# Kernel optimization log

Hardware: AMD Instinct MI355X
Metric: run time of the kernel (lower is better)

## Reference

```python
import jax, jax.numpy as jnp
import numpy as np

B_, L_, D_MODEL, N_LAYER, VOCAB = 4, 2048, 512, 2, 128
D_INNER, D_STATE, DT_RANK, D_CONV = 2 * D_MODEL, 16, D_MODEL // 16, 4
NDIR = 2  # forward / backward Mamba stacks


def setup_inputs() -> dict:
    key = jax.random.key(0)
    ks = jax.random.split(key, 12)
    f = jax.random.normal
    A_init = jnp.broadcast_to(
        jnp.log(jnp.arange(1, D_STATE + 1, dtype=jnp.float32)),
        (NDIR, N_LAYER, D_INNER, D_STATE)) + 0.0
    return {
        "input_ids": jax.random.randint(ks[0], (B_, L_), 0, VOCAB),
        "padding_mask": jnp.ones((B_, L_), dtype=bool),
        "embed": 0.02 * f(ks[1], (NDIR, VOCAB, D_MODEL)),
        "in_proj_w": 0.02 * f(ks[2], (NDIR, N_LAYER, 2 * D_INNER, D_MODEL)),
        "conv_w": 0.1 * f(ks[3], (NDIR, N_LAYER, D_INNER, 1, D_CONV)),
        "conv_b": 0.1 * f(ks[4], (NDIR, N_LAYER, D_INNER)),
        "x_proj_w": 0.02 * f(ks[5], (NDIR, N_LAYER, DT_RANK + 2 * D_STATE, D_INNER)),
        "dt_proj_w": 0.1 * f(ks[6], (NDIR, N_LAYER, D_INNER, DT_RANK)),
        "dt_proj_b": -4.0 + 0.5 * jax.random.uniform(ks[7], (NDIR, N_LAYER, D_INNER)),
        "A_log": A_init,
        "D": jnp.ones((NDIR, N_LAYER, D_INNER)),
        "out_proj_w": 0.02 * f(ks[8], (NDIR, N_LAYER, D_MODEL, D_INNER)),
        "norm_w": jnp.ones((NDIR, N_LAYER, D_MODEL)),
        "norm_f_w": jnp.ones((NDIR, D_MODEL)),
        "proj_w": 0.02 * f(ks[9], (D_MODEL, 2 * D_MODEL)),
        "proj_b": jnp.zeros((D_MODEL,)),
    }


def _rmsnorm(x, w, eps=1e-5):
    return x * jax.lax.rsqrt(jnp.mean(jnp.square(x), axis=-1, keepdims=True) + eps) * w


def _selective_scan(u, dt, Bm, Cm, A, Dp):
    # u, dt: (b, l, d_inner); Bm, Cm: (b, l, d_state)
    b, l, di = u.shape

    def step(h, inp):
        u_t, dt_t, b_t, c_t = inp                      # (b,di) (b,di) (b,n) (b,n)
        dA = jnp.exp(dt_t[:, :, None] * A)             # (b, di, n)
        h = dA * h + (dt_t * u_t)[:, :, None] * b_t[:, None, :]
        return h, jnp.einsum('bdn,bn->bd', h, c_t)

    h0 = jnp.zeros((b, di, A.shape[-1]), u.dtype)
    xs = (jnp.swapaxes(u, 0, 1), jnp.swapaxes(dt, 0, 1),
          jnp.swapaxes(Bm, 0, 1), jnp.swapaxes(Cm, 0, 1))
    _, ys = jax.lax.scan(step, h0, xs)                 # ys: (l, b, di)
    return jnp.swapaxes(ys, 0, 1) + u * Dp


def _mamba(x, p):
    in_w, cw, cb, xw, dtw, dtb, alog, dp, ow = p
    xz = jnp.einsum('bld,ed->ble', x, in_w)            # (b, l, 2*d_inner)
    u, z = jnp.split(xz, 2, axis=-1)
    uc = jnp.swapaxes(u, 1, 2)                         # (b, d_inner, l)
    uc = jax.lax.conv_general_dilated(
        uc, cw, (1,), [(D_CONV - 1, 0)], feature_group_count=D_INNER)
    u = jax.nn.silu(jnp.swapaxes(uc + cb[None, :, None], 1, 2))
    xdbl = jnp.einsum('bld,ed->ble', u, xw)
    dt, Bm, Cm = jnp.split(xdbl, [DT_RANK, DT_RANK + D_STATE], axis=-1)
    dt = jax.nn.softplus(jnp.einsum('blr,dr->bld', dt, dtw) + dtb)
    y = _selective_scan(u, dt, Bm, Cm, -jnp.exp(alog), dp)
    y = y * jax.nn.silu(z)
    return jnp.einsum('bld,ed->ble', y, ow)


def _mixer(ids, d, embed, in_proj_w, conv_w, conv_b, x_proj_w, dt_proj_w,
           dt_proj_b, A_log, D, out_proj_w, norm_w, norm_f_w):
    hidden = embed[d][ids]
    residual = None
    for i in range(N_LAYER):
        residual = hidden if residual is None else hidden + residual
        hidden = _rmsnorm(residual, norm_w[d, i])
        p = (in_proj_w[d, i], conv_w[d, i], conv_b[d, i], x_proj_w[d, i],
             dt_proj_w[d, i], dt_proj_b[d, i], A_log[d, i], D[d, i],
             out_proj_w[d, i])
        hidden = _mamba(hidden, p)
    return _rmsnorm(hidden + residual, norm_f_w[d])


def reference(input_ids, padding_mask, embed, in_proj_w, conv_w, conv_b,
              x_proj_w, dt_proj_w, dt_proj_b, A_log, D, out_proj_w, norm_w,
              norm_f_w, proj_w, proj_b):
    args = (embed, in_proj_w, conv_w, conv_b, x_proj_w, dt_proj_w, dt_proj_b,
            A_log, D, out_proj_w, norm_w, norm_f_w)
    fwd = _mixer(input_ids, 0, *args)
    bwd = jnp.flip(_mixer(jnp.flip(input_ids, 1), 1, *args), 1)
    out = jnp.concatenate([fwd, bwd], axis=-1)        # (b, l, 2*d_model)
    return jnp.einsum('ble,oe->blo', out, proj_w) + proj_b
```

## Files before the change

### kernel.cpp

```cpp
#include <hip/hip_runtime.h>
#include <hip/hip_bf16.h>

#define B_   4
#define L_   2048
#define DM   512
#define DI   1024
#define NST  16
#define DTR  32
#define ROWS  (B_ * L_)
#define ROWS2 (2 * ROWS)
#define NCHUNK 32
#define CLEN  (L_ / NCHUNK)
#define LN2R 1.4426950408889634f

typedef unsigned short u16;
typedef __attribute__((ext_vector_type(8))) short bf16x8;
typedef __attribute__((ext_vector_type(4))) float f32x4;
typedef __attribute__((ext_vector_type(4))) float float4v;
typedef __attribute__((ext_vector_type(2))) float f32x2;

__device__ __forceinline__ float bf2f(u16 h) {
  union { unsigned int u; float f; } v; v.u = ((unsigned int)h) << 16; return v.f;
}
__device__ __forceinline__ u16 f2bf(float f) {
  union { float f; unsigned int u; } v; v.f = f;
  unsigned int u = v.u;
  if ((u & 0x7fffffffu) > 0x7f800000u) return (u16)((u >> 16) | 0x0040u);
  return (u16)((u + 0x7fffu + ((u >> 16) & 1u)) >> 16);
}
__device__ __forceinline__ float sigmoidf_(float x) { return 1.f / (1.f + __expf(-x)); }

__device__ __forceinline__ f32x2 pk_mul(f32x2 a, f32x2 b) {
  f32x2 d; asm("v_pk_mul_f32 %0, %1, %2" : "=v"(d) : "v"(a), "v"(b)); return d;
}
__device__ __forceinline__ f32x2 pk_fma(f32x2 a, f32x2 b, f32x2 c) {
  f32x2 d; asm("v_pk_fma_f32 %0, %1, %2, %3" : "=v"(d) : "v"(a), "v"(b), "v"(c)); return d;
}

__device__ __forceinline__ void gload16(const u16* g, u16* l) {
  __builtin_amdgcn_global_load_lds(
      (const __attribute__((address_space(1))) void*)g,
      (__attribute__((address_space(3))) void*)l, 16, 0, 0);
}

__global__ __launch_bounds__(256) void cvt_k(const float* __restrict__ in,
                                             u16* __restrict__ out, int n4) {
  int i = blockIdx.x * 256 + threadIdx.x;
  if (i >= n4) return;
  float4v v = *(const float4v*)&in[i * 4];
  u16 o[4];
  o[0] = f2bf(v.x); o[1] = f2bf(v.y); o[2] = f2bf(v.z); o[3] = f2bf(v.w);
  *(ulong1*)&out[i * 4] = *(ulong1*)o;
}

__global__ __launch_bounds__(256) void trp_k(const float* __restrict__ in,
                                             float* __restrict__ out) {
  int o = blockIdx.x * 256 + threadIdx.x;
  int li = o >> 15;
  int k = (o >> 10) & (DTR - 1);
  int d = o & (DI - 1);
  out[o] = in[((size_t)li * DI + d) * DTR + k];
}

__global__ __launch_bounds__(256) void embed_k(const int* __restrict__ ids,
                                               const float* __restrict__ emb,
                                               float* __restrict__ res) {
  int idx = blockIdx.x * 256 + threadIdx.x;
  int c = idx & (DM - 1);
  int row = idx >> 9;
  int dir = row >> 13;
  int r = row & (ROWS - 1);
  int b = r >> 11;
  int l = r & (L_ - 1);
  int sl = dir ? (L_ - 1 - l) : l;
  int id = ids[(b << 11) + sl];
  res[idx] = emb[(size_t)dir * 128 * DM + id * DM + c];
}

template <bool ADD>
__global__ __launch_bounds__(256) void addnorm_k(float* __restrict__ res,
                                                 const float* __restrict__ hid,
                                                 const float* __restrict__ norm_w,
                                                 int layer,
                                                 u16* __restrict__ xn) {
  int row = blockIdx.x;
  int dir = row >> 13;
  const float* w = norm_w + (size_t)(dir * 2 + layer) * DM;
  int tid = threadIdx.x;
  int base = row * DM;
  float x0 = res[base + tid];
  float x1 = res[base + 256 + tid];
  if (ADD) {
    x0 += hid[base + tid];
    x1 += hid[base + 256 + tid];
    res[base + tid] = x0;
    res[base + 256 + tid] = x1;
  }
  float s = x0 * x0 + x1 * x1;
  for (int off = 32; off; off >>= 1) s += __shfl_xor(s, off);
  __shared__ float ps[4];
  if (!(tid & 63)) ps[tid >> 6] = s;
  __syncthreads();
  float tot = ps[0] + ps[1] + ps[2] + ps[3];
  float rs = 1.f / sqrtf(tot / (float)DM + 1e-5f);
  xn[base + tid]       = f2bf(x0 * rs * w[tid]);
  xn[base + 256 + tid] = f2bf(x1 * rs * w[tid + 256]);
}

#define MFMA_B16(a, b, c) __builtin_amdgcn_mfma_f32_16x16x32_bf16(a, b, c, 0, 0, 0)

__global__ __launch_bounds__(512) void gemm8p_k(const u16* __restrict__ A,
                                                const u16* __restrict__ W,
                                                u16* __restrict__ outU,
                                                u16* __restrict__ outZ,
                                                int K) {
  __shared__ u16 As[2][2][256 * 32];
  __shared__ u16 Wsh[2][2][256 * 32];
  int tid = threadIdx.x;
  int lane = tid & 63;
  int wv = tid >> 6;
  int wr = wv >> 2, wc = wv & 3;
  int bid = blockIdx.x;
  int xcd = bid & 7, jj = bid >> 3;
  int mt = xcd * 8 + (jj & 7);
  int nt = jj >> 3;
  int m0 = mt * 256, n0 = nt * 256;
  const u16* Weff = W + (size_t)(m0 >> 13) * (size_t)2 * (2 * DI) * DM;
  f32x4 acc[8][4];
#pragma unroll
  for (int i = 0; i < 8; ++i)
#pragma unroll
    for (int j = 0; j < 4; ++j) acc[i][j] = (f32x4){0.f, 0.f, 0.f, 0.f};
  int rr = lane & 15;
  int sl = lane >> 4;
  int pofs = ((sl + (rr >> 1)) & 3) * 8;
  int lr = lane >> 2;
  int ls = ((lane & 3) - (lr >> 1)) & 3;

  auto stA = [&](int tau, int ks) {
    int buf = tau & 1;
#pragma unroll
    for (int j = 0; j < 2; ++j)
      gload16(A + (size_t)(m0 + j * 128 + wv * 16 + lr) * K + tau * 64 + ks * 32 + ls * 8,
              &As[buf][ks][(j * 128 + wv * 16) * 32]);
  };
  auto stW = [&](int tau, int ks) {
    int buf = tau & 1;
#pragma unroll
    for (int j = 0; j < 2; ++j)
      gload16(Weff + (size_t)(n0 + j * 128 + wv * 16 + lr) * K + tau * 64 + ks * 32 + ls * 8,
              &Wsh[buf][ks][(j * 128 + wv * 16) * 32]);
  };

  int NT = K / 64;
  stA(0, 0); stW(0, 0); stA(0, 1); stW(0, 1);
  asm volatile("s_waitcnt vmcnt(4)" ::: "memory");
  __builtin_amdgcn_sched_barrier(0);
  __builtin_amdgcn_s_barrier();
  __builtin_amdgcn_sched_barrier(0);

  for (int tau = 0; tau < NT; ++tau) {
    int buf = tau & 1;
    bool more = (tau + 1 < NT);
    bf16x8 af[8], w0, w1;
#pragma unroll
    for (int mi = 0; mi < 8; ++mi)
      af[mi] = *(bf16x8*)&As[buf][0][(wr * 128 + mi * 16 + rr) * 32 + pofs];
    w0 = *(bf16x8*)&Wsh[buf][0][(wc * 64 + 0 * 16 + rr) * 32 + pofs];
    w1 = *(bf16x8*)&Wsh[buf][0][(wc * 64 + 1 * 16 + rr) * 32 + pofs];
    if (more) stA(tau + 1, 0);
    __builtin_amdgcn_sched_barrier(0);
    __builtin_amdgcn_s_barrier();
    asm volatile("s_waitcnt lgkmcnt(0)" ::: "memory");
    __builtin_amdgcn_sched_barrier(0);
    __builtin_amdgcn_s_setprio(1);
#pragma unroll
    for (int mi = 0; mi < 8; ++mi) {
      acc[mi][0] = MFMA_B16(af[mi], w0, acc[mi][0]);
      acc[mi][1] = MFMA_B16(af[mi], w1, acc[mi][1]);
    }
    __builtin_amdgcn_s_setprio(0);
    __builtin_amdgcn_s_barrier();
    __builtin_amdgcn_sched_barrier(0);
    w0 = *(bf16x8*)&Wsh[buf][0][(wc * 64 + 2 * 16 + rr) * 32 + pofs];
    w1 = *(bf16x8*)&Wsh[buf][0][(wc * 64 + 3 * 16 + rr) * 32 + pofs];
    if (more) {
      stW(tau + 1, 0);
      asm volatile("s_waitcnt vmcnt(4)" ::: "memory");
    } else {
      asm volatile("s_waitcnt vmcnt(0)" ::: "memory");
    }
    __builtin_amdgcn_sched_barrier(0);
    __builtin_amdgcn_s_barrier();
    asm volatile("s_waitcnt lgkmcnt(0)" ::: "memory");
    __builtin_amdgcn_sched_barrier(0);
    __builtin_amdgcn_s_setprio(1);
#pragma unroll
    for (int mi = 0; mi < 8; ++mi) {
      acc[mi][2] = MFMA_B16(af[mi], w0, acc[mi][2]);
      acc[mi][3] = MFMA_B16(af[mi], w1, acc[mi][3]);
    }
    __builtin_amdgcn_s_setprio(0);
    __builtin_amdgcn_s_barrier();
    __builtin_amdgcn_sched_barrier(0);
#pragma unroll
    for (int mi = 0; mi < 8; ++mi)
      af[mi] = *(bf16x8*)&As[buf][1][(wr * 128 + mi * 16 + rr) * 32 + pofs];
    w0 = *(bf16x8*)&Wsh[buf][1][(wc * 64 + 0 * 16 + rr) * 32 + pofs];
    w1 = *(bf16x8*)&Wsh[buf][1][(wc * 64 + 1 * 16 + rr) * 32 + pofs];
    if (more) stA(tau + 1, 1);
    __builtin_amdgcn_sched_barrier(0);
    __builtin_amdgcn_s_barrier();
    asm volatile("s_waitcnt lgkmcnt(0)" ::: "memory");
    __builtin_amdgcn_sched_barrier(0);
    __builtin_amdgcn_s_setprio(1);
#pragma unroll
    for (int mi = 0; mi < 8; ++mi) {
      acc[mi][0] = MFMA_B16(af[mi], w0, acc[mi][0]);
      acc[mi][1] = MFMA_B16(af[mi], w1, acc[mi][1]);
    }
    __builtin_amdgcn_s_setprio(0);
    __builtin_amdgcn_s_barrier();
    __builtin_amdgcn_sched_barrier(0);
    w0 = *(bf16x8*)&Wsh[buf][1][(wc * 64 + 2 * 16 + rr) * 32 + pofs];
    w1 = *(bf16x8*)&Wsh[buf][1][(wc * 64 + 3 * 16 + rr) * 32 + pofs];
    if (more) {
      stW(tau + 1, 1);
      asm volatile("s_waitcnt vmcnt(4)" ::: "memory");
    }
    __builtin_amdgcn_sched_barrier(0);
    __builtin_amdgcn_s_barrier();
    asm volatile("s_waitcnt lgkmcnt(0)" ::: "memory");
    __builtin_amdgcn_sched_barrier(0);
    __builtin_amdgcn_s_setprio(1);
#pragma unroll
    for (int mi = 0; mi < 8; ++mi) {
      acc[mi][2] = MFMA_B16(af[mi], w0, acc[mi][2]);
      acc[mi][3] = MFMA_B16(af[mi], w1, acc[mi][3]);
    }
    __builtin_amdgcn_s_setprio(0);
    __builtin_amdgcn_s_barrier();
    __builtin_amdgcn_sched_barrier(0);
  }
  int cr = (lane >> 4) << 2;
  int cc = lane & 15;
  u16* outp = (n0 < DI) ? outU : outZ;
  int cb0 = (n0 < DI) ? n0 : (n0 - DI);
#pragma unroll
  for (int mi = 0; mi < 8; ++mi)
#pragma unroll
    for (int ni = 0; ni < 4; ++ni) {
      int row = m0 + wr * 128 + mi * 16 + cr;
      int col = cb0 + wc * 64 + ni * 16 + cc;
#pragma unroll
      for (int j = 0; j < 4; ++j)
        outp[(size_t)(row + j) * DI + col] = f2bf(acc[mi][ni][j]);
    }
}

#define EPI_F32  0
#define EPI_BF16 1
#define EPI_BIAS 2

template <int BN, int EPI, int SK = 1>
__global__ __launch_bounds__(256) void gemm_bt(const u16* __restrict__ A,
                                               const u16* __restrict__ W,
                                               void* __restrict__ outp,
                                               const float* __restrict__ bias,
                                               int N, int K, size_t wsd) {
  constexpr int BM = 128, BK = 32;
  constexpr int NF = BN / 32;
  constexpr int G = (BN == 128) ? 4 : 3;
  __shared__ u16 As[4][BM * BK];
  __shared__ u16 Wsh[4][BN * BK];
  int tid = threadIdx.x;
  int lane = tid & 63;
  int wv = tid >> 6;
  int wr = wv >> 1, wc = wv & 1;
  int m0 = blockIdx.x * BM;
  int n0 = (SK > 1) ? 0 : blockIdx.y * BN;
  int koff = (SK > 1) ? blockIdx.y * (K / SK) : 0;
  int KS = K / SK;
  int NK = KS / BK;
  const u16* Weff = W + (size_t)(m0 >> 13) * wsd;
  f32x4 acc[4][NF];
#pragma unroll
  for (int i = 0; i < 4; ++i)
#pragma unroll
    for (int j = 0; j < NF; ++j) acc[i][j] = (f32x4){0.f, 0.f, 0.f, 0.f};
  int rr = lane & 15;
  int kk = (lane >> 4) << 3;
  int l4 = lane >> 2;
  int c8 = (lane & 3) << 3;
  const u16* Ag = A + (size_t)(m0 + l4) * K + koff + c8;
  const u16* Wg = Weff + (size_t)(n0 + l4) * K + koff + c8;

  auto stage = [&](int k0, int buf) {
    gload16(Ag + (size_t)(wv * 16) * K + k0, &As[buf][wv * 512]);
    gload16(Ag + (size_t)((wv + 4) * 16) * K + k0, &As[buf][(wv + 4) * 512]);
    gload16(Wg + (size_t)(wv * 16) * K + k0, &Wsh[buf][wv * 512]);
    if (BN == 128)
      gload16(Wg + (size_t)((wv + 4) * 16) * K + k0, &Wsh[buf][(wv + 4) * 512]);
  };

  stage(0, 0); stage(BK, 1); stage(2 * BK, 2);
  for (int k = 0; k < NK; ++k) {
    if (k < NK - 2)
      asm volatile("s_waitcnt vmcnt(%0)" :: "n"(2 * G) : "memory");
    else if (k == NK - 2)
      asm volatile("s_waitcnt vmcnt(%0)" :: "n"(G) : "memory");
    else
      asm volatile("s_waitcnt vmcnt(0)" ::: "memory");
    __builtin_amdgcn_s_barrier();
    __builtin_amdgcn_sched_barrier(0);
    if (k + 3 < NK) stage((k + 3) * BK, (k + 3) & 3);
    __builtin_amdgcn_sched_barrier(0);
    int cur = k & 3;
    bf16x8 af[4], wf[NF];
#pragma unroll
    for (int mi = 0; mi < 4; ++mi)
      af[mi] = *(bf16x8*)&As[cur][(wr * 64 + mi * 16 + rr) * BK + kk];
#pragma unroll
    for (int ni = 0; ni < NF; ++ni)
      wf[ni] = *(bf16x8*)&Wsh[cur][(wc * (BN / 2) + ni * 16 + rr) * BK + kk];
#pragma unroll
    for (int mi = 0; mi < 4; ++mi)
#pragma unroll
      for (int ni = 0; ni < NF; ++ni)
        acc[mi][ni] = __builtin_amdgcn_mfma_f32_16x16x32_bf16(af[mi], wf[ni], acc[mi][ni], 0, 0, 0);
  }
  int cr = (lane >> 4) << 2;
  int cc = lane & 15;
  float* outF = (float*)outp +
      ((SK > 1) ? (size_t)blockIdx.y * (size_t)gridDim.x * BM * N : 0);
#pragma unroll
  for (int mi = 0; mi < 4; ++mi)
#pragma unroll
    for (int ni = 0; ni < NF; ++ni) {
      int row = m0 + wr * 64 + mi * 16 + cr;
      int col = n0 + wc * (BN / 2) + ni * 16 + cc;
      float bv = (EPI == EPI_BIAS) ? bias[col] : 0.f;
#pragma unroll
      for (int j = 0; j < 4; ++j) {
        float v = acc[mi][ni][j] + bv;
        if (EPI == EPI_BF16)
          ((u16*)outp)[(size_t)(row + j) * N + col] = f2bf(v);
        else
          outF[(size_t)(row + j) * N + col] = v;
      }
    }
}

__global__ __launch_bounds__(256) void conv_k(const u16* __restrict__ xzu,
                                              const float* __restrict__ conv_w,
                                              const float* __restrict__ conv_b,
                                              int layer,
                                              u16* __restrict__ uh) {
  int idx = blockIdx.x * 256 + threadIdx.x;
  int c = idx & (DI - 1);
  int row = idx >> 10;
  int dir = row >> 13;
  int l = row & (L_ - 1);
  const float* cw = conv_w + (size_t)(dir * 2 + layer) * DI * 4;
  const float* cb = conv_b + (size_t)(dir * 2 + layer) * DI;
  float acc = cb[c];
#pragma unroll
  for (int j = 0; j < 4; ++j) {
    int ls = l + j - 3;
    if (ls >= 0)
      acc += bf2f(xzu[(size_t)(row + j - 3) * DI + c]) * cw[c * 4 + j];
  }
  float s = acc * sigmoidf_(acc);
  uh[idx] = f2bf(s);
}

__device__ __forceinline__ bool a_fast(const float* alog, int d, float& a20) {
  a20 = -__expf(alog[d * NST]) * LN2R;
  bool fast = true;
#pragma unroll
  for (int n = 1; n < NST; ++n) {
    float an = -__expf(alog[d * NST + n]) * LN2R;
    fast &= (fabsf(an - (float)(n + 1) * a20) <= 1e-5f * (float)(n + 1) * fabsf(a20));
  }
  return fast;
}

__device__ __forceinline__ void stage_xs(float (*xs)[64], const float* xp,
                                         size_t rowbase, int tid) {
  size_t base = rowbase * 64;
  const float4v* s0 = (const float4v*)(xp + base);
  const float4v* s1 = (const float4v*)(xp + (size_t)ROWS2 * 64 + base);
  const float4v* s2 = (const float4v*)(xp + (size_t)2 * ROWS2 * 64 + base);
  const float4v* s3 = (const float4v*)(xp + (size_t)3 * ROWS2 * 64 + base);
  float4v* dst = (float4v*)&xs[0][0];
#pragma unroll
  for (int i = 0; i < CLEN / 16; ++i)
    dst[tid + i * 256] = s0[tid + i * 256] + s1[tid + i * 256] +
                         s2[tid + i * 256] + s3[tid + i * 256];
}

__device__ __forceinline__ float dt_of(const float (*xs)[64], int t,
                                       const f32x2* w2, float bias) {
  f32x2 a2 = {bias, 0.f};
  const f32x2* xr2 = (const f32x2*)&xs[t][0];
#pragma unroll
  for (int j = 0; j < 16; ++j) a2 = pk_fma(xr2[j], w2[j], a2);
  float a = a2.x + a2.y;
  return (a > 15.f) ? a : __logf(1.f + __expf(a));
}

__global__ __launch_bounds__(256) void dtscan1_k(u16* uS,
                                                 const float* __restrict__ xp,
                                                 const float* __restrict__ dtw_t,
                                                 const float* __restrict__ dtb,
                                                 const float* __restrict__ alog_,
                                                 const float* __restrict__ Dp,
                                                 int layer,
                                                 u16* __restrict__ ylg,
                                                 float* __restrict__ chk) {
  __shared__ float xs[CLEN][64];
  int blk = blockIdx.x;
  int db = blk & 3;
  int c  = (blk >> 2) & (NCHUNK - 1);
  int nb = blk >> 7;
  int dir = nb >> 2;
  int tid = threadIdx.x;
  int d  = db * 256 + tid;
  int li = dir * 2 + layer;
  const float* dtwT = dtw_t + (size_t)li * DTR * DI;
  const float* alog = alog_ + (size_t)li * DI * NST;
  int t0 = c * CLEN;
  size_t rowbase = (size_t)nb * L_ + t0;
  stage_xs(xs, xp, rowbase, tid);
  f32x2 w2[16];
#pragma unroll
  for (int j = 0; j < 16; ++j)
    w2[j] = (f32x2){dtwT[(size_t)(2 * j) * DI + d], dtwT[(size_t)(2 * j + 1) * DI + d]};
  float bias = dtb[(size_t)li * DI + d];
  float Dv = Dp[(size_t)li * DI + d];
  float a20;
  bool fast = a_fast(alog, d, a20);
  __syncthreads();
  float S = 0.f;
  size_t ubase = rowbase * DI + d;
  f32x2 h2[8];
#pragma unroll
  for (int q = 0; q < 8; ++q) h2[q] = (f32x2){0.f, 0.f};
  for (int t = 0; t < CLEN; ++t) {
    float dtv = dt_of(xs, t, w2, bias);
    float uv = bf2f(uS[ubase]);
    float du = dtv * uv;
    S += dtv;
    f32x2 acc2 = {0.f, 0.f};
    if (fast) {
      float p1 = exp2f(dtv * a20);
      float p2 = p1 * p1;
      f32x2 pw = {p1, p2};
      f32x2 pst = {p2, p2};
      f32x2 du2 = {du, du};
#pragma unroll
      for (int k = 0; k < 4; ++k) {
        f32x4 bv = *(const f32x4*)&xs[t][DTR + k * 4];
        f32x4 cv = *(const f32x4*)&xs[t][DTR + NST + k * 4];
        f32x2 blo = __builtin_shufflevector(bv, bv, 0, 1);
        f32x2 bhi = __builtin_shufflevector(bv, bv, 2, 3);
        f32x2 clo = __builtin_shufflevector(cv, cv, 0, 1);
        f32x2 chi = __builtin_shufflevector(cv, cv, 2, 3);
        h2[2 * k]     = pk_fma(pw, h2[2 * k], pk_mul(du2, blo));
        acc2          = pk_fma(h2[2 * k], clo, acc2);
        pw = pk_mul(pw, pst);
        h2[2 * k + 1] = pk_fma(pw, h2[2 * k + 1], pk_mul(du2, bhi));
        acc2          = pk_fma(h2[2 * k + 1], chi, acc2);
        if (k < 3) pw = pk_mul(pw, pst);
      }
    } else {
#pragma unroll
      for (int q = 0; q < 8; ++q) {
        float e0 = exp2f(dtv * -__expf(alog[d * NST + 2 * q]) * LN2R);
        float e1 = exp2f(dtv * -__expf(alog[d * NST + 2 * q + 1]) * LN2R);
        f32x2 bv = *(const f32x2*)&xs[t][DTR + q * 2];
        f32x2 cv = *(const f32x2*)&xs[t][DTR + NST + q * 2];
        h2[q] = pk_fma((f32x2){e0, e1}, h2[q], pk_mul((f32x2){du, du}, bv));
        acc2 = pk_fma(h2[q], cv, acc2);
      }
    }
    float yloc = acc2.x + acc2.y + uv * Dv;
    ylg[ubase] = f2bf(yloc);
    uS[ubase]  = f2bf(S);
    ubase += DI;
  }
  const size_t H = (size_t)8 * NCHUNK * DI * NST;
  size_t idx = ((size_t)(nb * NCHUNK + c) * DI + d) * NST;
#pragma unroll
  for (int n = 0; n < NST; ++n) {
    float an = -__expf(alog[d * NST + n]) * LN2R;
    chk[idx + n]     = exp2f(an * S);
    chk[H + idx + n] = (n & 1) ? h2[n >> 1].y : h2[n >> 1].x;
  }
}

__global__ __launch_bounds__(256) void scan2_k(float* __restrict__ chk) {
  int j = blockIdx.x * 256 + threadIdx.x;
  int n = j & 15;
  int d = (j >> 4) & (DI - 1);
  int nb = j >> 14;
  const size_t H = (size_t)8 * NCHUNK * DI * NST;
  float h = 0.f;
  for (int c = 0; c < NCHUNK; ++c) {
    size_t idx = ((size_t)(nb * NCHUNK + c) * DI + d) * NST + n;
    float a = chk[idx];
    float hl = chk[H + idx];
    chk[H + idx] = h;
    h = a * h + hl;
  }
}

__global__ __launch_bounds__(256) void scan3lite_k(const u16* __restrict__ uS,
                                                   const float* __restrict__ xp,
                                                   const float* __restrict__ alog_,
                                                   int layer,
                                                   const float* __restrict__ chk,
                                                   const u16* __restrict__ xzz,
                                                   u16* ylg) {
  __shared__ float xc[CLEN][NST];
  int blk = blockIdx.x;
  int db = blk & 3;
  int c  = (blk >> 2) & (NCHUNK - 1);
  int nb = blk >> 7;
  int dir = nb >> 2;
  int tid = threadIdx.x;
  int d  = db * 256 + tid;
  int li = dir * 2 + layer;
  const float* alog = alog_ + (size_t)li * DI * NST;
  int t0 = c * CLEN;
  size_t rowbase = (size_t)nb * L_ + t0;
  {
    int r = tid >> 2, v = tid & 3;
    size_t base = (rowbase + r) * 64 + DTR + NST + v * 4;
    float4v s = *(const float4v*)(xp + base)
              + *(const float4v*)(xp + (size_t)ROWS2 * 64 + base)
              + *(const float4v*)(xp + (size_t)2 * ROWS2 * 64 + base)
              + *(const float4v*)(xp + (size_t)3 * ROWS2 * 64 + base);
    *(float4v*)&xc[r][v * 4] = s;
  }
  float a20;
  bool fast = a_fast(alog, d, a20);
  const size_t H = (size_t)8 * NCHUNK * DI * NST;
  size_t cidx = ((size_t)(nb * NCHUNK + c) * DI + d) * NST;
  f32x2 h2[8];
#pragma unroll
  for (int q = 0; q < 8; ++q) h2[q] = *(const f32x2*)&chk[H + cidx + 2 * q];
  float A2g[NST];
  if (!fast) {
#pragma unroll
    for (int n = 0; n < NST; ++n) A2g[n] = -__expf(alog[d * NST + n]) * LN2R;
  }
  __syncthreads();
  size_t ubase = rowbase * DI + d;
  for (int t = 0; t < CLEN; ++t) {
    float S = bf2f(uS[ubase]);
    f32x2 corr2 = {0.f, 0.f};
    if (fast) {
      float w1 = exp2f(a20 * S);
      float w2_ = w1 * w1;
      f32x2 pw = {w1, w2_};
      f32x2 pst = {w2_, w2_};
#pragma unroll
      for (int q = 0; q < 8; ++q) {
        f32x2 cp = *(const f32x2*)&xc[t][2 * q];
        corr2 = pk_fma(pk_mul(pw, h2[q]), cp, corr2);
        if (q < 7) pw = pk_mul(pw, pst);
      }
    } else {
#pragma unroll
      for (int q = 0; q < 8; ++q) {
        f32x2 e = {exp2f(A2g[2 * q] * S), exp2f(A2g[2 * q + 1] * S)};
        f32x2 cp = *(const f32x2*)&xc[t][2 * q];
        corr2 = pk_fma(pk_mul(e, h2[q]), cp, corr2);
      }
    }
    float y = bf2f(ylg[ubase]) + corr2.x + corr2.y;
    float z = bf2f(xzz[ubase]);
    ylg[ubase] = f2bf(y * z * sigmoidf_(z));
    ubase += DI;
  }
}

__global__ __launch_bounds__(256) void fincat_k(const float* __restrict__ hid,
                                                const float* __restrict__ res,
                                                const float* __restrict__ norm_f,
                                                u16* __restrict__ cat) {
  int row = blockIdx.x;
  int dir = row >> 13;
  const float* w = norm_f + (size_t)dir * DM;
  int tid = threadIdx.x;
  int base = row * DM;
  float x0 = hid[base + tid] + res[base + tid];
  float x1 = hid[base + 256 + tid] + res[base + 256 + tid];
  float s = x0 * x0 + x1 * x1;
  for (int off = 32; off; off >>= 1) s += __shfl_xor(s, off);
  __shared__ float ps[4];
  if (!(tid & 63)) ps[tid >> 6] = s;
  __syncthreads();
  float tot = ps[0] + ps[1] + ps[2] + ps[3];
  float rs = 1.f / sqrtf(tot / (float)DM + 1e-5f);
  int r = row & (ROWS - 1);
  int b = r >> 11, l = r & (L_ - 1);
  size_t drow = dir ? ((size_t)(b << 11) + (L_ - 1 - l)) : (size_t)r;
  size_t obase = drow * (2 * DM) + (size_t)dir * DM;
  cat[obase + tid]       = f2bf(x0 * rs * w[tid]);
  cat[obase + 256 + tid] = f2bf(x1 * rs * w[tid + 256]);
}

extern "C" void kernel_launch(void* const* d_in, const int* in_sizes, int n_in,
                              void* d_out, int out_size, void* d_ws, size_t ws_size,
                              hipStream_t stream) {
  const int*   ids      = (const int*)d_in[0];
  const float* embed    = (const float*)d_in[2];
  const float* in_w     = (const float*)d_in[3];
  const float* conv_w   = (const float*)d_in[4];
  const float* conv_b   = (const float*)d_in[5];
  const float* x_w      = (const float*)d_in[6];
  const float* dt_w     = (const float*)d_in[7];
  const float* dt_bias  = (const float*)d_in[8];
  const float* A_log    = (const float*)d_in[9];
  const float* Dp       = (const float*)d_in[10];
  const float* out_w    = (const float*)d_in[11];
  const float* norm_w   = (const float*)d_in[12];
  const float* norm_f   = (const float*)d_in[13];
  const float* proj_w   = (const float*)d_in[14];
  const float* proj_b   = (const float*)d_in[15];

  char* ws = (char*)d_ws;
  size_t off = 0;
  auto alloc = [&](size_t bytes) {
    void* p = ws + off;
    off += (bytes + 255) & ~(size_t)255;
    return p;
  };
  float* res  = (float*)alloc((size_t)ROWS2 * DM * 4);
  float* hid  = (float*)alloc((size_t)ROWS2 * DM * 4);
  u16*   xnyg = (u16*)alloc((size_t)ROWS2 * DI * 2);
  u16*   xzz  = (u16*)alloc((size_t)ROWS2 * DI * 2);
  void*  shrd = alloc((size_t)ROWS2 * DI * 2);
  u16*   u_h  = (u16*)alloc((size_t)ROWS2 * DI * 2);
  const int N_IN  = 4 * 2 * DI * DM;
  const int N_XW  = 4 * 64 * DI;
  const int N_OW  = 4 * DM * DI;
  const int N_PW  = DM * 2 * DM;
  const int N_DTW = 4 * DTR * DI;
  u16*   in_wb  = (u16*)alloc((size_t)N_IN * 2);
  u16*   x_wb   = (u16*)alloc((size_t)N_XW * 2);
  u16*   out_wb = (u16*)alloc((size_t)N_OW * 2);
  u16*   pr_wb  = (u16*)alloc((size_t)N_PW * 2);
  float* dtw_t  = (float*)alloc((size_t)N_DTW * 4);
  if (off > ws_size) return;

  u16*   xzu = (u16*)shrd;
  float* chk = (float*)shrd;
  u16*   cat = (u16*)shrd;

  cvt_k<<<(N_IN / 4 + 255) / 256, 256, 0, stream>>>(in_w, in_wb, N_IN / 4);
  cvt_k<<<(N_XW / 4 + 255) / 256, 256, 0, stream>>>(x_w, x_wb, N_XW / 4);
  cvt_k<<<(N_OW / 4 + 255) / 256, 256, 0, stream>>>(out_w, out_wb, N_OW / 4);
  cvt_k<<<(N_PW / 4 + 255) / 256, 256, 0, stream>>>(proj_w, pr_wb, N_PW / 4);
  trp_k<<<N_DTW / 256, 256, 0, stream>>>(dt_w, dtw_t);

  embed_k<<<ROWS2 * DM / 256, 256, 0, stream>>>(ids, embed, res);
  for (int i = 0; i < 2; ++i) {
    if (i == 0)
      addnorm_k<false><<<ROWS2, 256, 0, stream>>>(res, hid, norm_w, i, xnyg);
    else
      addnorm_k<true><<<ROWS2, 256, 0, stream>>>(res, hid, norm_w, i, xnyg);
    gemm8p_k<<<512, 512, 0, stream>>>(
        xnyg, in_wb + (size_t)i * 2 * DI * DM, xzu, xzz, DM);
    conv_k<<<ROWS2 * DI / 256, 256, 0, stream>>>(xzu, conv_w, conv_b, i, u_h);
    gemm_bt<64, EPI_F32, 4><<<dim3(ROWS2 / 128, 4), 256, 0, stream>>>(
        u_h, x_wb + (size_t)i * 64 * DI, hid, nullptr, 64, DI, (size_t)2 * 64 * DI);
    dtscan1_k<<<1024, 256, 0, stream>>>(u_h, hid, dtw_t, dt_bias, A_log, Dp, i,
                                        xnyg, chk);
    scan2_k<<<512, 256, 0, stream>>>(chk);
    scan3lite_k<<<1024, 256, 0, stream>>>(u_h, hid, A_log, i, chk, xzz, xnyg);
    gemm_bt<64, EPI_F32><<<dim3(ROWS2 / 128, DM / 64), 256, 0, stream>>>(
        xnyg, out_wb + (size_t)i * DM * DI, hid, nullptr, DM, DI, (size_t)2 * DM * DI);
  }
  fincat_k<<<ROWS2, 256, 0, stream>>>(hid, res, norm_f, cat);
  gemm_bt<64, EPI_BIAS><<<dim3(ROWS / 128, DM / 64), 256, 0, stream>>>(
      cat, pr_wb, (float*)d_out, proj_b, DM, DI, 0);
}
```

Measured before the change: 771.1 us.

## Simplify in_proj GEMM pipeline and break scan dependency chains

```diff
diff --git a/kernel.cpp b/kernel.cpp
--- a/kernel.cpp
+++ b/kernel.cpp
@@ -109,13 +109,13 @@
 
 #define MFMA_B16(a, b, c) __builtin_amdgcn_mfma_f32_16x16x32_bf16(a, b, c, 0, 0, 0)
 
-__global__ __launch_bounds__(512) void gemm8p_k(const u16* __restrict__ A,
-                                                const u16* __restrict__ W,
-                                                u16* __restrict__ outU,
-                                                u16* __restrict__ outZ,
-                                                int K) {
-  __shared__ u16 As[2][2][256 * 32];
-  __shared__ u16 Wsh[2][2][256 * 32];
+__global__ __launch_bounds__(512) void g256_k(const u16* __restrict__ A,
+                                              const u16* __restrict__ W,
+                                              u16* __restrict__ outU,
+                                              u16* __restrict__ outZ,
+                                              int K) {
+  __shared__ u16 As[2][256 * 32];
+  __shared__ u16 Wsh[2][256 * 32];
   int tid = threadIdx.x;
   int lane = tid & 63;
   int wv = tid >> 6;
@@ -137,108 +137,45 @@
   int lr = lane >> 2;
   int ls = ((lane & 3) - (lr >> 1)) & 3;
 
-  auto stA = [&](int tau, int ks) {
+  auto stage = [&](int tau, int buf) {
+#pragma unroll
+    for (int j = 0; j < 2; ++j) {
+      gload16(A + (size_t)(m0 + j * 128 + wv * 16 + lr) * K + tau * 32 + ls * 8,
+              &As[buf][(j * 128 + wv * 16) * 32]);
+      gload16(Weff + (size_t)(n0 + j * 128 + wv * 16 + lr) * K + tau * 32 + ls * 8,
+              &Wsh[buf][(j * 128 + wv * 16) * 32]);
+    }
+  };
+
+  int NK = K / 32;
+  stage(0, 0);
+  for (int tau = 0; tau < NK; ++tau) {
     int buf = tau & 1;
-#pragma unroll
-    for (int j = 0; j < 2; ++j)
-      gload16(A + (size_t)(m0 + j * 128 + wv * 16 + lr) * K + tau * 64 + ks * 32 + ls * 8,
-              &As[buf][ks][(j * 128 + wv * 16) * 32]);
-  };
-  auto stW = [&](int tau, int ks) {
-    int buf = tau & 1;
-#pragma unroll
-    for (int j = 0; j < 2; ++j)
-      gload16(Weff + (size_t)(n0 + j * 128 + wv * 16 + lr) * K + tau * 64 + ks * 32 + ls * 8,
-              &Wsh[buf][ks][(j * 128 + wv * 16) * 32]);
-  };
-
-  int NT = K / 64;
-  stA(0, 0); stW(0, 0); stA(0, 1); stW(0, 1);
-  asm volatile("s_waitcnt vmcnt(4)" ::: "memory");
-  __builtin_amdgcn_sched_barrier(0);
-  __builtin_amdgcn_s_barrier();
-  __builtin_amdgcn_sched_barrier(0);
-
-  for (int tau = 0; tau < NT; ++tau) {
-    int buf = tau & 1;
-    bool more = (tau + 1 < NT);
-    bf16x8 af[8], w0, w1;
-#pragma unroll
-    for (int mi = 0; mi < 8; ++mi)
-      af[mi] = *(bf16x8*)&As[buf][0][(wr * 128 + mi * 16 + rr) * 32 + pofs];
-    w0 = *(bf16x8*)&Wsh[buf][0][(wc * 64 + 0 * 16 + rr) * 32 + pofs];
-    w1 = *(bf16x8*)&Wsh[buf][0][(wc * 64 + 1 * 16 + rr) * 32 + pofs];
-    if (more) stA(tau + 1, 0);
+    bool more = (tau + 1 < NK);
+    if (more) stage(tau + 1, buf ^ 1);
+    if (more)
+      asm volatile("s_waitcnt vmcnt(4)" ::: "memory");
+    else
+      asm volatile("s_waitcnt vmcnt(0)" ::: "memory");
     __builtin_amdgcn_sched_barrier(0);
     __builtin_amdgcn_s_barrier();
+    __builtin_amdgcn_sched_barrier(0);
+    bf16x8 af[8], wf[4];
+#pragma unroll
+    for (int mi = 0; mi < 8; ++mi)
+      af[mi] = *(bf16x8*)&As[buf][(wr * 128 + mi * 16 + rr) * 32 + pofs];
+#pragma unroll
+    for (int ni = 0; ni < 4; ++ni)
+      wf[ni] = *(bf16x8*)&Wsh[buf][(wc * 64 + ni * 16 + rr) * 32 + pofs];
+    __builtin_amdgcn_s_setprio(1);
+#pragma unroll
+    for (int mi = 0; mi < 8; ++mi)
+#pragma unroll
+      for (int ni = 0; ni < 4; ++ni)
+        acc[mi][ni] = MFMA_B16(af[mi], wf[ni], acc[mi][ni]);
+    __builtin_amdgcn_s_setprio(0);
     asm volatile("s_waitcnt lgkmcnt(0)" ::: "memory");
     __builtin_amdgcn_sched_barrier(0);
-    __builtin_amdgcn_s_setprio(1);
-#pragma unroll
-    for (int mi = 0; mi < 8; ++mi) {
-      acc[mi][0] = MFMA_B16(af[mi], w0, acc[mi][0]);
-      acc[mi][1] = MFMA_B16(af[mi], w1, acc[mi][1]);
-    }
-    __builtin_amdgcn_s_setprio(0);
-    __builtin_amdgcn_s_barrier();
-    __builtin_amdgcn_sched_barrier(0);
-    w0 = *(bf16x8*)&Wsh[buf][0][(wc * 64 + 2 * 16 + rr) * 32 + pofs];
-    w1 = *(bf16x8*)&Wsh[buf][0][(wc * 64 + 3 * 16 + rr) * 32 + pofs];
-    if (more) {
-      stW(tau + 1, 0);
-      asm volatile("s_waitcnt vmcnt(4)" ::: "memory");
-    } else {
-      asm volatile("s_waitcnt vmcnt(0)" ::: "memory");
-    }
-    __builtin_amdgcn_sched_barrier(0);
-    __builtin_amdgcn_s_barrier();
-    asm volatile("s_waitcnt lgkmcnt(0)" ::: "memory");
-    __builtin_amdgcn_sched_barrier(0);
-    __builtin_amdgcn_s_setprio(1);
-#pragma unroll
-    for (int mi = 0; mi < 8; ++mi) {
-      acc[mi][2] = MFMA_B16(af[mi], w0, acc[mi][2]);
-      acc[mi][3] = MFMA_B16(af[mi], w1, acc[mi][3]);
-    }
-    __builtin_amdgcn_s_setprio(0);
-    __builtin_amdgcn_s_barrier();
-    __builtin_amdgcn_sched_barrier(0);
-#pragma unroll
-    for (int mi = 0; mi < 8; ++mi)
-      af[mi] = *(bf16x8*)&As[buf][1][(wr * 128 + mi * 16 + rr) * 32 + pofs];
-    w0 = *(bf16x8*)&Wsh[buf][1][(wc * 64 + 0 * 16 + rr) * 32 + pofs];
-    w1 = *(bf16x8*)&Wsh[buf][1][(wc * 64 + 1 * 16 + rr) * 32 + pofs];
-    if (more) stA(tau + 1, 1);
-    __builtin_amdgcn_sched_barrier(0);
-    __builtin_amdgcn_s_barrier();
-    asm volatile("s_waitcnt lgkmcnt(0)" ::: "memory");
-    __builtin_amdgcn_sched_barrier(0);
-    __builtin_amdgcn_s_setprio(1);
-#pragma unroll
-    for (int mi = 0; mi < 8; ++mi) {
-      acc[mi][0] = MFMA_B16(af[mi], w0, acc[mi][0]);
-      acc[mi][1] = MFMA_B16(af[mi], w1, acc[mi][1]);
-    }
-    __builtin_amdgcn_s_setprio(0);
-    __builtin_amdgcn_s_barrier();
-    __builtin_amdgcn_sched_barrier(0);
-    w0 = *(bf16x8*)&Wsh[buf][1][(wc * 64 + 2 * 16 + rr) * 32 + pofs];
-    w1 = *(bf16x8*)&Wsh[buf][1][(wc * 64 + 3 * 16 + rr) * 32 + pofs];
-    if (more) {
-      stW(tau + 1, 1);
-      asm volatile("s_waitcnt vmcnt(4)" ::: "memory");
-    }
-    __builtin_amdgcn_sched_barrier(0);
-    __builtin_amdgcn_s_barrier();
-    asm volatile("s_waitcnt lgkmcnt(0)" ::: "memory");
-    __builtin_amdgcn_sched_barrier(0);
-    __builtin_amdgcn_s_setprio(1);
-#pragma unroll
-    for (int mi = 0; mi < 8; ++mi) {
-      acc[mi][2] = MFMA_B16(af[mi], w0, acc[mi][2]);
-      acc[mi][3] = MFMA_B16(af[mi], w1, acc[mi][3]);
-    }
-    __builtin_amdgcn_s_setprio(0);
     __builtin_amdgcn_s_barrier();
     __builtin_amdgcn_sched_barrier(0);
   }
@@ -401,11 +338,16 @@
 
 __device__ __forceinline__ float dt_of(const float (*xs)[64], int t,
                                        const f32x2* w2, float bias) {
-  f32x2 a2 = {bias, 0.f};
-  const f32x2* xr2 = (const f32x2*)&xs[t][0];
-#pragma unroll
-  for (int j = 0; j < 16; ++j) a2 = pk_fma(xr2[j], w2[j], a2);
-  float a = a2.x + a2.y;
+  const f32x2* x = (const f32x2*)&xs[t][0];
+  f32x2 a0 = {bias, 0.f}, a1 = {0.f, 0.f}, a2 = {0.f, 0.f}, a3 = {0.f, 0.f};
+#pragma unroll
+  for (int j = 0; j < 4; ++j) {
+    a0 = pk_fma(x[4 * j],     w2[4 * j],     a0);
+    a1 = pk_fma(x[4 * j + 1], w2[4 * j + 1], a1);
+    a2 = pk_fma(x[4 * j + 2], w2[4 * j + 2], a2);
+    a3 = pk_fma(x[4 * j + 3], w2[4 * j + 3], a3);
+  }
+  float a = (a0.x + a0.y) + (a1.x + a1.y) + ((a2.x + a2.y) + (a3.x + a3.y));
   return (a > 15.f) ? a : __logf(1.f + __expf(a));
 }
 
@@ -446,12 +388,13 @@
   f32x2 h2[8];
 #pragma unroll
   for (int q = 0; q < 8; ++q) h2[q] = (f32x2){0.f, 0.f};
+  float uv = bf2f(uS[ubase]);
   for (int t = 0; t < CLEN; ++t) {
+    float uv_nx = (t + 1 < CLEN) ? bf2f(uS[ubase + DI]) : 0.f;
     float dtv = dt_of(xs, t, w2, bias);
-    float uv = bf2f(uS[ubase]);
     float du = dtv * uv;
     S += dtv;
-    f32x2 acc2 = {0.f, 0.f};
+    f32x2 accA = {0.f, 0.f}, accB = {0.f, 0.f};
     if (fast) {
       float p1 = exp2f(dtv * a20);
       float p2 = p1 * p1;
@@ -467,10 +410,10 @@
         f32x2 clo = __builtin_shufflevector(cv, cv, 0, 1);
         f32x2 chi = __builtin_shufflevector(cv, cv, 2, 3);
         h2[2 * k]     = pk_fma(pw, h2[2 * k], pk_mul(du2, blo));
-        acc2          = pk_fma(h2[2 * k], clo, acc2);
+        accA          = pk_fma(h2[2 * k], clo, accA);
         pw = pk_mul(pw, pst);
         h2[2 * k + 1] = pk_fma(pw, h2[2 * k + 1], pk_mul(du2, bhi));
-        acc2          = pk_fma(h2[2 * k + 1], chi, acc2);
+        accB          = pk_fma(h2[2 * k + 1], chi, accB);
         if (k < 3) pw = pk_mul(pw, pst);
       }
     } else {
@@ -481,12 +424,14 @@
         f32x2 bv = *(const f32x2*)&xs[t][DTR + q * 2];
         f32x2 cv = *(const f32x2*)&xs[t][DTR + NST + q * 2];
         h2[q] = pk_fma((f32x2){e0, e1}, h2[q], pk_mul((f32x2){du, du}, bv));
-        acc2 = pk_fma(h2[q], cv, acc2);
+        if (q & 1) accB = pk_fma(h2[q], cv, accB);
+        else       accA = pk_fma(h2[q], cv, accA);
       }
     }
-    float yloc = acc2.x + acc2.y + uv * Dv;
+    float yloc = (accA.x + accA.y) + (accB.x + accB.y) + uv * Dv;
     ylg[ubase] = f2bf(yloc);
     uS[ubase]  = f2bf(S);
+    uv = uv_nx;
     ubase += DI;
   }
   const size_t H = (size_t)8 * NCHUNK * DI * NST;
@@ -557,9 +502,10 @@
   }
   __syncthreads();
   size_t ubase = rowbase * DI + d;
+  float S = bf2f(uS[ubase]);
   for (int t = 0; t < CLEN; ++t) {
-    float S = bf2f(uS[ubase]);
-    f32x2 corr2 = {0.f, 0.f};
+    float S_nx = (t + 1 < CLEN) ? bf2f(uS[ubase + DI]) : 0.f;
+    f32x2 corrA = {0.f, 0.f}, corrB = {0.f, 0.f};
     if (fast) {
       float w1 = exp2f(a20 * S);
       float w2_ = w1 * w1;
@@ -568,7 +514,8 @@
 #pragma unroll
       for (int q = 0; q < 8; ++q) {
         f32x2 cp = *(const f32x2*)&xc[t][2 * q];
-        corr2 = pk_fma(pk_mul(pw, h2[q]), cp, corr2);
+        if (q & 1) corrB = pk_fma(pk_mul(pw, h2[q]), cp, corrB);
+        else       corrA = pk_fma(pk_mul(pw, h2[q]), cp, corrA);
         if (q < 7) pw = pk_mul(pw, pst);
       }
     } else {
@@ -576,12 +523,14 @@
       for (int q = 0; q < 8; ++q) {
         f32x2 e = {exp2f(A2g[2 * q] * S), exp2f(A2g[2 * q + 1] * S)};
         f32x2 cp = *(const f32x2*)&xc[t][2 * q];
-        corr2 = pk_fma(pk_mul(e, h2[q]), cp, corr2);
+        if (q & 1) corrB = pk_fma(pk_mul(e, h2[q]), cp, corrB);
+        else       corrA = pk_fma(pk_mul(e, h2[q]), cp, corrA);
       }
     }
-    float y = bf2f(ylg[ubase]) + corr2.x + corr2.y;
+    float y = bf2f(ylg[ubase]) + (corrA.x + corrA.y) + (corrB.x + corrB.y);
     float z = bf2f(xzz[ubase]);
     ylg[ubase] = f2bf(y * z * sigmoidf_(z));
+    S = S_nx;
     ubase += DI;
   }
 }
@@ -672,7 +621,7 @@
       addnorm_k<false><<<ROWS2, 256, 0, stream>>>(res, hid, norm_w, i, xnyg);
     else
       addnorm_k<true><<<ROWS2, 256, 0, stream>>>(res, hid, norm_w, i, xnyg);
-    gemm8p_k<<<512, 512, 0, stream>>>(
+    g256_k<<<512, 512, 0, stream>>>(
         xnyg, in_wb + (size_t)i * 2 * DI * DM, xzu, xzz, DM);
     conv_k<<<ROWS2 * DI / 256, 256, 0, stream>>>(xzu, conv_w, conv_b, i, u_h);
     gemm_bt<64, EPI_F32, 4><<<dim3(ROWS2 / 128, 4), 256, 0, stream>>>(
```

Result: faster. 750.7 us (-2.6%).
